# Kernel optimization log

Measured on AMD Instinct MI355X. Metric: run time of the kernel, lower is better.

The kernel has to match this reference:

```python
import jax, jax.numpy as jnp
import numpy as np

DIST = 3.0
COEFF = 10.0
NEG_SLOPE = 0.3  # keras LeakyReLU default


def _probe_points(dist=DIST):
    # fixed 26 probe offsets on a sphere of radius `dist` (from build())
    angles = np.array(
        [[j * 0.125 - 0.125, i * 0.125 + (j - 1) * 0.0625] for j in range(3) for i in range(8)]
        + [[-0.25, 0.0], [0.25, 0.0]],
        dtype=np.float32,
    ) * (2.0 * np.pi)
    a, b = angles[:, 0], angles[:, 1]
    pts = np.stack([np.sin(a), np.cos(a) * np.cos(b), np.cos(a) * np.sin(b)], axis=-1) * dist
    return jnp.asarray(pts, dtype=jnp.float32)  # (26, 3)


def setup_inputs() -> dict:
    key = jax.random.key(0)
    k1, k2, k3 = jax.random.split(key, 3)
    B, n, f = 2, 1024, 3
    m, out_feats, num_convs = 26, 6, 5
    points = jax.random.normal(k1, (B, n, 3 + f), dtype=jnp.float32)
    # per-conv Dense(m*f -> out_feats) weights/bias, stacked over num_convs
    W = jax.random.normal(k2, (num_convs, m * f, out_feats), dtype=jnp.float32) * 0.1
    b = jax.random.normal(k3, (num_convs, out_feats), dtype=jnp.float32) * 0.1
    return {"points": points, "W": W, "b": b}


def reference(points, W, b):
    B, n, df = points.shape
    d = 3
    f = df - d
    probes = _probe_points()              # (m, d)
    m = probes.shape[0]
    coords = points[..., :d]              # (B, n, d) -> centers too (l = n)
    feats = points[..., d:]               # (B, n, f)
    centers = coords
    # probes per center: (B, l, m, d)
    probes_per_center = centers[:, :, None, :] + probes[None, None, :, :]
    # delta: (B, l, m, n, d)
    delta = coords[:, None, None, :, :] - probes_per_center[:, :, :, None, :]
    sq = jnp.sum(delta * delta, axis=-1)  # (B, l, m, n)
    wgt = COEFF / (sq + COEFF)            # inverse-distance weights
    # weighted feature sum: (B, l, m, f), averaged over n
    wf = jnp.einsum('blmn,bnf->blmf', wgt, feats) / n
    x = wf.reshape(B, n, m * f)           # (B, l, m*f)
    # num_convs parallel Dense + LeakyReLU (Dropout is identity at inference)
    h = jnp.einsum('blx,kxo->blko', x, W) + b[None, None, :, :]
    h = jnp.where(h > 0, h, NEG_SLOPE * h)
    convs = h.reshape(B, n, -1)           # (B, n, num_convs*out_feats)
    return jnp.concatenate([centers, convs], axis=-1)  # (B, n, 3 + 30)
```

## Files before the change

kernel.cpp:

```cpp
#include <hip/hip_runtime.h>


#define NPTS   1024
#define COEFF  10.0f
#define NEG    0.3f

typedef float  v2f __attribute__((ext_vector_type(2)));
typedef __fp16 h2  __attribute__((ext_vector_type(2)));

#define CA 4.24264068f
#define CY 3.91968890f
#define CZ 1.62358830f

constexpr int M0[14] = {0,5, 1,4, 2,3, 7,6, 8,12, 10,14, 24,25};
constexpr int M1[12] = {16,19, 17,18, 20,23, 21,22, 9,13, 11,15};

__device__ __forceinline__ v2f pk_fma(v2f a, v2f b, v2f c) {
  v2f d;
  asm("v_pk_fma_f32 %0, %1, %2, %3" : "=v"(d) : "v"(a), "v"(b), "v"(c));
  return d;
}
__device__ __forceinline__ v2f pk_fma_n(v2f a, v2f b, v2f c) {
  v2f d;
  asm("v_pk_fma_f32 %0, %1, %2, %3 neg_lo:[1,0,0] neg_hi:[1,0,0]"
      : "=v"(d) : "v"(a), "v"(b), "v"(c));
  return d;
}
__device__ __forceinline__ v2f pk_add(v2f a, v2f b) {
  v2f d;
  asm("v_pk_add_f32 %0, %1, %2" : "=v"(d) : "v"(a), "v"(b));
  return d;
}
__device__ __forceinline__ v2f pk_sub(v2f a, v2f b) {
  v2f d;
  asm("v_pk_add_f32 %0, %1, %2 neg_lo:[0,1] neg_hi:[0,1]"
      : "=v"(d) : "v"(a), "v"(b));
  return d;
}

#define DPP_H2(x, ctrl, rm, bm, bc)                                          \
  x = x + __builtin_bit_cast(h2, __builtin_amdgcn_update_dpp(                \
      0, __builtin_bit_cast(int, x), ctrl, rm, bm, bc))

__device__ __forceinline__ h2 h2_wave_sum_to_lane63(h2 x) {
  DPP_H2(x, 0x111, 0xf, 0xf, true);
  DPP_H2(x, 0x112, 0xf, 0xf, true);
  DPP_H2(x, 0x114, 0xf, 0xe, false);
  DPP_H2(x, 0x118, 0xf, 0xc, false);
  DPP_H2(x, 0x142, 0xa, 0xf, false);
  DPP_H2(x, 0x143, 0xc, 0xf, false);
  return x;
}

__device__ __forceinline__ void rcp8_cvt(const v2f* t, h2* wp) {
  const float p0 = t[0].x * t[0].y, p1 = t[1].x * t[1].y;
  const float p2 = t[2].x * t[2].y, p3 = t[3].x * t[3].y;
  const float q01 = p0 * p1, q23 = p2 * p3;
  const float r   = __builtin_amdgcn_rcpf(q01 * q23);
  const float r01 = q23 * r, r23 = q01 * r;
  const float i0 = p1 * r01, i1 = p0 * r01;
  const float i2 = p3 * r23, i3 = p2 * r23;
  wp[0] = __builtin_amdgcn_cvt_pkrtz(t[0].y * i0, t[0].x * i0);
  wp[1] = __builtin_amdgcn_cvt_pkrtz(t[1].y * i1, t[1].x * i1);
  wp[2] = __builtin_amdgcn_cvt_pkrtz(t[2].y * i2, t[2].x * i2);
  wp[3] = __builtin_amdgcn_cvt_pkrtz(t[3].y * i3, t[3].x * i3);
}
__device__ __forceinline__ void rcp4_cvt(const v2f* t, h2* wp) {
  const float p0 = t[0].x * t[0].y, p1 = t[1].x * t[1].y;
  const float r  = __builtin_amdgcn_rcpf(p0 * p1);
  const float i0 = p1 * r, i1 = p0 * r;
  wp[0] = __builtin_amdgcn_cvt_pkrtz(t[0].y * i0, t[0].x * i0);
  wp[1] = __builtin_amdgcn_cvt_pkrtz(t[1].y * i1, t[1].x * i1);
}

template <int HALF>
__device__ void run_main(const float* __restrict__ soa, int lane,
                         v2f cxp, v2f cyp, v2f czp, float* acc) {
  constexpr int NP = HALF ? 12 : 14;
  const v2f kCA = {CA, CA}, kCY = {CY, CY}, kCZ = {CZ, CZ};
  const v2f k6 = {6.f, 6.f}, k19 = {19.f, 19.f};

  for (int it = 0; it < 8; ++it) {
    const int nb = it * 128 + 2 * lane;
    const v2f pxp = *reinterpret_cast<const v2f*>(&soa[0 * NPTS + nb]);
    const v2f pyp = *reinterpret_cast<const v2f*>(&soa[1 * NPTS + nb]);
    const v2f pzp = *reinterpret_cast<const v2f*>(&soa[2 * NPTS + nb]);
    const v2f f0v = *reinterpret_cast<const v2f*>(&soa[3 * NPTS + nb]);
    const v2f f1v = *reinterpret_cast<const v2f*>(&soa[4 * NPTS + nb]);
    const v2f f2v = *reinterpret_cast<const v2f*>(&soa[5 * NPTS + nb]);

    const v2f dx = pk_sub(pxp, cxp);
    const v2f dy = pk_sub(pyp, cyp);
    const v2f dz = pk_sub(pzp, czp);
    v2f base = pk_fma(dz, dz, k19);
    base = pk_fma(dy, dy, base);
    base = pk_fma(dx, dx, base);

    v2f t[NP];
    if constexpr (HALF == 0) {
      const v2f rx = pk_fma(kCA, dx, base);
      const v2f sA = pk_fma  (kCZ, dz, rx);
      const v2f sB = pk_fma_n(kCZ, dz, rx);
      const v2f sC = pk_fma_n(kCY, dz, rx);
      const v2f sD = pk_fma  (kCY, dz, rx);
      t[0]  = pk_fma_n(kCY, dy, sA);  t[1]  = pk_fma(kCY, dy, sA);
      t[2]  = pk_fma_n(kCY, dy, sB);  t[3]  = pk_fma(kCY, dy, sB);
      t[4]  = pk_fma_n(kCZ, dy, sC);  t[5]  = pk_fma(kCZ, dy, sC);
      t[6]  = pk_fma_n(kCZ, dy, sD);  t[7]  = pk_fma(kCZ, dy, sD);
      t[8]  = pk_fma_n(k6, dy, base); t[9]  = pk_fma(k6, dy, base);
      t[10] = pk_fma_n(k6, dz, base); t[11] = pk_fma(k6, dz, base);
      t[12] = pk_fma  (k6, dx, base); t[13] = pk_fma_n(k6, dx, base);
    } else {
      const v2f rx = pk_fma_n(kCA, dx, base);
      const v2f sA = pk_fma_n(kCZ, dz, rx);
      const v2f sB = pk_fma_n(kCY, dz, rx);
      const v2f sC = pk_fma  (kCZ, dz, rx);
      const v2f sD = pk_fma  (kCY, dz, rx);
      const v2f u = pk_add(dy, dz), v = pk_sub(dy, dz);
      t[0]  = pk_fma_n(kCY, dy, sA);  t[1]  = pk_fma(kCY, dy, sA);
      t[2]  = pk_fma_n(kCZ, dy, sB);  t[3]  = pk_fma(kCZ, dy, sB);
      t[4]  = pk_fma  (kCY, dy, sC);  t[5]  = pk_fma_n(kCY, dy, sC);
      t[6]  = pk_fma  (kCZ, dy, sD);  t[7]  = pk_fma_n(kCZ, dy, sD);
      t[8]  = pk_fma_n(kCA, u, base); t[9]  = pk_fma(kCA, u, base);
      t[10] = pk_fma  (kCA, v, base); t[11] = pk_fma_n(kCA, v, base);
    }

    h2 wp[NP];
    rcp8_cvt(t + 0, wp + 0);
    rcp8_cvt(t + 4, wp + 4);
    rcp8_cvt(t + 8, wp + 8);
    if constexpr (NP == 14) rcp4_cvt(t + 12, wp + 12);

    const h2 f0p = __builtin_amdgcn_cvt_pkrtz(f0v.x, f0v.y);
    const h2 f1p = __builtin_amdgcn_cvt_pkrtz(f1v.x, f1v.y);
    const h2 f2p = __builtin_amdgcn_cvt_pkrtz(f2v.x, f2v.y);

    #pragma unroll
    for (int j = 0; j < NP; ++j) {
      acc[j * 3 + 0] = __builtin_amdgcn_fdot2(wp[j], f0p, acc[j * 3 + 0], false);
      acc[j * 3 + 1] = __builtin_amdgcn_fdot2(wp[j], f1p, acc[j * 3 + 1], false);
      acc[j * 3 + 2] = __builtin_amdgcn_fdot2(wp[j], f2p, acc[j * 3 + 2], false);
    }
  }
}

template <int HALF>
__device__ __forceinline__ void reduce_store(float* acc, int lane, float* sx) {
  constexpr int NP = HALF ? 12 : 14;
  constexpr int NH = NP * 3 / 2;
  h2 red[NH];
  #pragma unroll
  for (int p = 0; p < NH; ++p)
    red[p] = __builtin_amdgcn_cvt_pkrtz(acc[2 * p], acc[2 * p + 1]);
  #pragma unroll
  for (int p = 0; p < NH; ++p)
    red[p] = h2_wave_sum_to_lane63(red[p]);
  if (lane == 63) {
    #pragma unroll
    for (int p = 0; p < NH; ++p) {
      const int a0 = 2 * p, a1 = 2 * p + 1;
      const int m0 = (HALF ? M1[a0 / 3] : M0[a0 / 3]);
      const int m1 = (HALF ? M1[a1 / 3] : M0[a1 / 3]);
      sx[m0 * 3 + a0 % 3] = (float)red[p].x;
      sx[m1 * 3 + a1 % 3] = (float)red[p].y;
    }
  }
}

__global__ __launch_bounds__(256, 4) void crossconv_kernel(
    const float* __restrict__ points,
    const float* __restrict__ W,
    const float* __restrict__ bias,
    float* __restrict__ out)
{
    __shared__ __align__(16) float soa[6 * NPTS];
    __shared__ __align__(16) float sx[2][80];

    const int tid    = threadIdx.x;
    const int lane   = tid & 63;
    const int w      = tid >> 6;
    const int cLocal = w >> 1;
    const int half   = w & 1;
    const int G      = blockIdx.x * 2 + cLocal;

    const float* batch = points + (G >> 10) * (NPTS * 6);

    {
      const float4* src4 = reinterpret_cast<const float4*>(batch) + 6 * tid;
      const float4 q0 = src4[0], q1 = src4[1], q2 = src4[2];
      const float4 q3 = src4[3], q4 = src4[4], q5 = src4[5];
      const int r = 4 * tid;
      soa[0*NPTS + r+0] = q0.x; soa[1*NPTS + r+0] = q0.y; soa[2*NPTS + r+0] = q0.z;
      soa[3*NPTS + r+0] = q0.w; soa[4*NPTS + r+0] = q1.x; soa[5*NPTS + r+0] = q1.y;
      soa[0*NPTS + r+1] = q1.z; soa[1*NPTS + r+1] = q1.w; soa[2*NPTS + r+1] = q2.x;
      soa[3*NPTS + r+1] = q2.y; soa[4*NPTS + r+1] = q2.z; soa[5*NPTS + r+1] = q2.w;
      soa[0*NPTS + r+2] = q3.x; soa[1*NPTS + r+2] = q3.y; soa[2*NPTS + r+2] = q3.z;
      soa[3*NPTS + r+2] = q3.w; soa[4*NPTS + r+2] = q4.x; soa[5*NPTS + r+2] = q4.y;
      soa[0*NPTS + r+3] = q4.z; soa[1*NPTS + r+3] = q4.w; soa[2*NPTS + r+3] = q5.x;
      soa[3*NPTS + r+3] = q5.y; soa[4*NPTS + r+3] = q5.z; soa[5*NPTS + r+3] = q5.w;
    }
    __syncthreads();

    const int   ci = ((blockIdx.x & 511) << 1) | cLocal;
    const float cx = soa[0*NPTS + ci], cy = soa[1*NPTS + ci], cz = soa[2*NPTS + ci];
    const v2f cxp = {cx, cx}, cyp = {cy, cy}, czp = {cz, cz};

    float acc[42];
    #pragma unroll
    for (int j = 0; j < 42; ++j) acc[j] = 0.f;

    if (half == 0) run_main<0>(soa, lane, cxp, cyp, czp, acc);
    else           run_main<1>(soa, lane, cxp, cyp, czp, acc);

    if (half == 0) reduce_store<0>(acc, lane, sx[cLocal]);
    else           reduce_store<1>(acc, lane, sx[cLocal]);
    __syncthreads();

    if (half == 0) {
      const float scale = COEFF / (float)NPTS;
      float* orow = out + G * 33;
      if (lane < 30) {
        const int k = lane / 6, o = lane % 6;
        const float* Wk = W + k * (78 * 6) + o;
        float h0 = 0.f, h1 = 0.f, h2_ = 0.f, h3 = 0.f;
        const float4* sxv = reinterpret_cast<const float4*>(sx[cLocal]);
        #pragma unroll
        for (int t4 = 0; t4 < 19; ++t4) {
          const float4 v = sxv[t4];
          h0  = fmaf(v.x, Wk[(t4 * 4 + 0) * 6], h0);
          h1  = fmaf(v.y, Wk[(t4 * 4 + 1) * 6], h1);
          h2_ = fmaf(v.z, Wk[(t4 * 4 + 2) * 6], h2_);
          h3  = fmaf(v.w, Wk[(t4 * 4 + 3) * 6], h3);
        }
        const float2 vt = *reinterpret_cast<const float2*>(&sx[cLocal][76]);
        h0 = fmaf(vt.x, Wk[76 * 6], h0);
        h1 = fmaf(vt.y, Wk[77 * 6], h1);
        const float dot = (h0 + h2_) + (h1 + h3);
        float h = fmaf(dot, scale, bias[lane]);
        h = (h > 0.f) ? h : NEG * h;
        orow[3 + lane] = h;
      } else if (lane < 33) {
        orow[lane - 30] = (lane == 30) ? cx : ((lane == 31) ? cy : cz);
      }
    }
}

extern "C" void kernel_launch(void* const* d_in, const int* in_sizes, int n_in,
                              void* d_out, int out_size, void* d_ws, size_t ws_size,
                              hipStream_t stream) {
    const float* points = (const float*)d_in[0];
    const float* W      = (const float*)d_in[1];
    const float* bias   = (const float*)d_in[2];
    float* out          = (float*)d_out;
    crossconv_kernel<<<1024, 256, 0, stream>>>(points, W, bias, out);
}
```

Before: 21.44 us.

## Store features as packed fp16 in LDS and double-buffer point loads

```diff
diff --git a/kernel.cpp b/kernel.cpp
--- a/kernel.cpp
+++ b/kernel.cpp
@@ -74,24 +74,37 @@
 }
 
 template <int HALF>
-__device__ void run_main(const float* __restrict__ soa, int lane,
-                         v2f cxp, v2f cyp, v2f czp, float* acc) {
+__device__ void run_main(const float* __restrict__ sxyz,
+                         const h2* __restrict__ sfeat,
+                         int lane, v2f cxp, v2f cyp, v2f czp, float* acc) {
   constexpr int NP = HALF ? 12 : 14;
   const v2f kCA = {CA, CA}, kCY = {CY, CY}, kCZ = {CZ, CZ};
   const v2f k6 = {6.f, 6.f}, k19 = {19.f, 19.f};
 
+  v2f px[2], py[2], pz[2];
+  h2  f0[2], f1[2], f2[2];
+
+#define LOADIT(buf, it)                                                       \
+  {                                                                           \
+    const int nb = (it) * 128 + 2 * lane;                                     \
+    const int nh = (it) * 64 + lane;                                          \
+    px[buf] = *reinterpret_cast<const v2f*>(&sxyz[0 * NPTS + nb]);            \
+    py[buf] = *reinterpret_cast<const v2f*>(&sxyz[1 * NPTS + nb]);            \
+    pz[buf] = *reinterpret_cast<const v2f*>(&sxyz[2 * NPTS + nb]);            \
+    f0[buf] = sfeat[0 * (NPTS / 2) + nh];                                     \
+    f1[buf] = sfeat[1 * (NPTS / 2) + nh];                                     \
+    f2[buf] = sfeat[2 * (NPTS / 2) + nh];                                     \
+  }
+
+  LOADIT(0, 0);
+  #pragma unroll
   for (int it = 0; it < 8; ++it) {
-    const int nb = it * 128 + 2 * lane;
-    const v2f pxp = *reinterpret_cast<const v2f*>(&soa[0 * NPTS + nb]);
-    const v2f pyp = *reinterpret_cast<const v2f*>(&soa[1 * NPTS + nb]);
-    const v2f pzp = *reinterpret_cast<const v2f*>(&soa[2 * NPTS + nb]);
-    const v2f f0v = *reinterpret_cast<const v2f*>(&soa[3 * NPTS + nb]);
-    const v2f f1v = *reinterpret_cast<const v2f*>(&soa[4 * NPTS + nb]);
-    const v2f f2v = *reinterpret_cast<const v2f*>(&soa[5 * NPTS + nb]);
-
-    const v2f dx = pk_sub(pxp, cxp);
-    const v2f dy = pk_sub(pyp, cyp);
-    const v2f dz = pk_sub(pzp, czp);
+    const int cur = it & 1, nxt = cur ^ 1;
+    if (it < 7) LOADIT(nxt, it + 1);
+
+    const v2f dx = pk_sub(px[cur], cxp);
+    const v2f dy = pk_sub(py[cur], cyp);
+    const v2f dz = pk_sub(pz[cur], czp);
     v2f base = pk_fma(dz, dz, k19);
     base = pk_fma(dy, dy, base);
     base = pk_fma(dx, dx, base);
@@ -131,17 +144,14 @@
     rcp8_cvt(t + 8, wp + 8);
     if constexpr (NP == 14) rcp4_cvt(t + 12, wp + 12);
 
-    const h2 f0p = __builtin_amdgcn_cvt_pkrtz(f0v.x, f0v.y);
-    const h2 f1p = __builtin_amdgcn_cvt_pkrtz(f1v.x, f1v.y);
-    const h2 f2p = __builtin_amdgcn_cvt_pkrtz(f2v.x, f2v.y);
-
     #pragma unroll
     for (int j = 0; j < NP; ++j) {
-      acc[j * 3 + 0] = __builtin_amdgcn_fdot2(wp[j], f0p, acc[j * 3 + 0], false);
-      acc[j * 3 + 1] = __builtin_amdgcn_fdot2(wp[j], f1p, acc[j * 3 + 1], false);
-      acc[j * 3 + 2] = __builtin_amdgcn_fdot2(wp[j], f2p, acc[j * 3 + 2], false);
+      acc[j * 3 + 0] = __builtin_amdgcn_fdot2(wp[j], f0[cur], acc[j * 3 + 0], false);
+      acc[j * 3 + 1] = __builtin_amdgcn_fdot2(wp[j], f1[cur], acc[j * 3 + 1], false);
+      acc[j * 3 + 2] = __builtin_amdgcn_fdot2(wp[j], f2[cur], acc[j * 3 + 2], false);
     }
   }
+#undef LOADIT
 }
 
 template <int HALF>
@@ -173,7 +183,8 @@
     const float* __restrict__ bias,
     float* __restrict__ out)
 {
-    __shared__ __align__(16) float soa[6 * NPTS];
+    __shared__ __align__(16) float sxyz[3 * NPTS];
+    __shared__ __align__(16) h2    sfeat[3 * NPTS / 2];
     __shared__ __align__(16) float sx[2][80];
 
     const int tid    = threadIdx.x;
@@ -190,27 +201,30 @@
       const float4 q0 = src4[0], q1 = src4[1], q2 = src4[2];
       const float4 q3 = src4[3], q4 = src4[4], q5 = src4[5];
       const int r = 4 * tid;
-      soa[0*NPTS + r+0] = q0.x; soa[1*NPTS + r+0] = q0.y; soa[2*NPTS + r+0] = q0.z;
-      soa[3*NPTS + r+0] = q0.w; soa[4*NPTS + r+0] = q1.x; soa[5*NPTS + r+0] = q1.y;
-      soa[0*NPTS + r+1] = q1.z; soa[1*NPTS + r+1] = q1.w; soa[2*NPTS + r+1] = q2.x;
-      soa[3*NPTS + r+1] = q2.y; soa[4*NPTS + r+1] = q2.z; soa[5*NPTS + r+1] = q2.w;
-      soa[0*NPTS + r+2] = q3.x; soa[1*NPTS + r+2] = q3.y; soa[2*NPTS + r+2] = q3.z;
-      soa[3*NPTS + r+2] = q3.w; soa[4*NPTS + r+2] = q4.x; soa[5*NPTS + r+2] = q4.y;
-      soa[0*NPTS + r+3] = q4.z; soa[1*NPTS + r+3] = q4.w; soa[2*NPTS + r+3] = q5.x;
-      soa[3*NPTS + r+3] = q5.y; soa[4*NPTS + r+3] = q5.z; soa[5*NPTS + r+3] = q5.w;
+      sxyz[0*NPTS + r+0] = q0.x; sxyz[1*NPTS + r+0] = q0.y; sxyz[2*NPTS + r+0] = q0.z;
+      sxyz[0*NPTS + r+1] = q1.z; sxyz[1*NPTS + r+1] = q1.w; sxyz[2*NPTS + r+1] = q2.x;
+      sxyz[0*NPTS + r+2] = q3.x; sxyz[1*NPTS + r+2] = q3.y; sxyz[2*NPTS + r+2] = q3.z;
+      sxyz[0*NPTS + r+3] = q4.z; sxyz[1*NPTS + r+3] = q4.w; sxyz[2*NPTS + r+3] = q5.x;
+      const int h = r >> 1;
+      sfeat[0*(NPTS/2) + h+0] = __builtin_amdgcn_cvt_pkrtz(q0.w, q2.y);
+      sfeat[0*(NPTS/2) + h+1] = __builtin_amdgcn_cvt_pkrtz(q3.w, q5.y);
+      sfeat[1*(NPTS/2) + h+0] = __builtin_amdgcn_cvt_pkrtz(q1.x, q2.z);
+      sfeat[1*(NPTS/2) + h+1] = __builtin_amdgcn_cvt_pkrtz(q4.x, q5.z);
+      sfeat[2*(NPTS/2) + h+0] = __builtin_amdgcn_cvt_pkrtz(q1.y, q2.w);
+      sfeat[2*(NPTS/2) + h+1] = __builtin_amdgcn_cvt_pkrtz(q4.y, q5.w);
     }
     __syncthreads();
 
     const int   ci = ((blockIdx.x & 511) << 1) | cLocal;
-    const float cx = soa[0*NPTS + ci], cy = soa[1*NPTS + ci], cz = soa[2*NPTS + ci];
+    const float cx = sxyz[0*NPTS + ci], cy = sxyz[1*NPTS + ci], cz = sxyz[2*NPTS + ci];
     const v2f cxp = {cx, cx}, cyp = {cy, cy}, czp = {cz, cz};
 
     float acc[42];
     #pragma unroll
     for (int j = 0; j < 42; ++j) acc[j] = 0.f;
 
-    if (half == 0) run_main<0>(soa, lane, cxp, cyp, czp, acc);
-    else           run_main<1>(soa, lane, cxp, cyp, czp, acc);
+    if (half == 0) run_main<0>(sxyz, sfeat, lane, cxp, cyp, czp, acc);
+    else           run_main<1>(sxyz, sfeat, lane, cxp, cyp, czp, acc);
 
     if (half == 0) reduce_store<0>(acc, lane, sx[cLocal]);
     else           reduce_store<1>(acc, lane, sx[cLocal]);
```

Result: no change. 21.27 us (median of 2 runs) (-0.8%).
